# Kernel tuning notes

Hardware: AMD Instinct MI355X
Metric: run time of the kernel (lower is better)

The kernel has to match this reference:

```python
import jax, jax.numpy as jnp
import numpy as np

# Dimensions
B = 256        # number of graphs
NPG = 128      # nodes per graph (max_nodes; uniform -> to_dense_batch == reshape)
H = 8          # num_heads
DH = 32        # head_dim
HID = H * DH   # hidden_dim = 256
E = 524288     # n_edges
NGT = 20       # num_gate_types
EF = 8         # edge_feat_dim


def setup_inputs() -> dict:
    key = jax.random.key(0)
    ks = jax.random.split(key, 20)
    n_nodes = B * NPG
    x = jax.random.normal(ks[0], (n_nodes, HID), jnp.float32)
    # edges stay within the source node's graph
    src = jax.random.randint(ks[1], (E,), 0, n_nodes, dtype=jnp.int32)
    dst = (src // NPG) * NPG + jax.random.randint(ks[2], (E,), 0, NPG, dtype=jnp.int32)
    edge_index = jnp.stack([src, dst])  # [2, E]
    edge_attr = jax.random.normal(ks[3], (E, EF), jnp.float32)
    edge_gate_type = jax.random.randint(ks[4], (E,), 0, NGT, dtype=jnp.int32)
    batch = (jnp.arange(n_nodes) // NPG).astype(jnp.int32)

    s = 1.0 / np.sqrt(HID)
    def lin(k, din, dout, scale):
        kw, kb = jax.random.split(k)
        return (jax.random.uniform(kw, (din, dout), jnp.float32, -scale, scale),
                jax.random.uniform(kb, (dout,), jnp.float32, -scale, scale))
    Wq, bq = lin(ks[5], HID, HID, s)
    Wk, bk = lin(ks[6], HID, HID, s)
    Wv, bv = lin(ks[7], HID, HID, s)
    Wo, bo = lin(ks[8], HID, HID, s)
    gate_table = jax.random.normal(ks[9], (NGT, H), jnp.float32)
    We, be = lin(ks[10], EF, H, 1.0 / np.sqrt(EF))
    return {"x": x, "edge_attr": edge_attr, "Wq": Wq, "bq": bq, "Wk": Wk, "bk": bk,
            "Wv": Wv, "bv": bv, "Wo": Wo, "bo": bo, "gate_table": gate_table,
            "We": We, "be": be, "edge_index": edge_index,
            "edge_gate_type": edge_gate_type, "batch": batch}


def _edge_bias(edge_index, edge_attr, edge_gate_type, batch, gate_table, We, be):
    src, dst = edge_index[0], edge_index[1]
    eb = batch[src]                       # edge -> graph id
    src_l = src - eb * NPG                # local node index within graph
    dst_l = dst - eb * NPG
    total = gate_table[edge_gate_type] + edge_attr @ We + be   # [E, H]
    bias = jnp.zeros((B, H, NPG, NPG), edge_attr.dtype)
    bias = bias.at[eb, :, src_l, dst_l].add(total)             # forward direction
    rev = jnp.where((src_l != dst_l)[:, None], total, 0.0)     # skip self-loops
    bias = bias.at[eb, :, dst_l, src_l].add(rev)               # reverse direction
    return bias


def reference(x, edge_attr, Wq, bq, Wk, bk, Wv, bv, Wo, bo, gate_table, We, be,
              edge_index, edge_gate_type, batch):
    scale = 1.0 / np.sqrt(DH)
    xd = x.reshape(B, NPG, HID)  # uniform graph sizes -> to_dense_batch is a reshape
    Q = (xd @ Wq + bq).reshape(B, NPG, H, DH).transpose(0, 2, 1, 3)  # [B,H,N,D]
    K = (xd @ Wk + bk).reshape(B, NPG, H, DH).transpose(0, 2, 1, 3)
    V = (xd @ Wv + bv).reshape(B, NPG, H, DH).transpose(0, 2, 1, 3)
    scores = jnp.einsum('bhqd,bhkd->bhqk', Q, K) * scale
    scores = scores + _edge_bias(edge_index, edge_attr, edge_gate_type, batch,
                                 gate_table, We, be)
    attn = jax.nn.softmax(scores, axis=-1)  # node_mask all-True (uniform sizes)
    out = jnp.einsum('bhqk,bhkd->bhqd', attn, V)
    out = out.transpose(0, 2, 1, 3).reshape(B * NPG, HID)
    return out @ Wo + bo
```

## Files before the change

### kernel.cpp

```cpp
#include <hip/hip_runtime.h>
#include <hip/hip_fp16.h>

typedef unsigned short u16;
typedef unsigned int u32;
typedef __attribute__((ext_vector_type(8))) short short8;
typedef __attribute__((ext_vector_type(4))) float f32x4;

#define MFMA16(a, b, c) __builtin_amdgcn_mfma_f32_16x16x32_bf16((a), (b), (c), 0, 0, 0)

#define ESTRIDE 2304

__device__ __forceinline__ float b2f(u16 u) {
  union { float f; unsigned int i; } v;
  v.i = ((unsigned int)u) << 16;
  return v.f;
}
__device__ __forceinline__ u16 f2b(float f) {
  union { float f; unsigned int i; } v;
  v.f = f;
  unsigned int x = v.i;
  return (u16)((x + 0x7FFFu + ((x >> 16) & 1u)) >> 16);
}
__device__ __forceinline__ u16 f2h_bits(float f) {
  __half h = __float2half(f);
  u16 b;
  __builtin_memcpy(&b, &h, 2);
  return b;
}
__device__ __forceinline__ float h2f_bits(u16 b) {
  __half h;
  __builtin_memcpy(&h, &b, 2);
  return __half2float(h);
}

__device__ __forceinline__ void gload_lds16(const u16* g, u16* l) {
  __builtin_amdgcn_global_load_lds(
      (const __attribute__((address_space(1))) void*)g,
      (__attribute__((address_space(3))) void*)l, 16, 0, 0);
}

__global__ __launch_bounds__(256) void cvt_wtrans_kernel(
    const float* __restrict__ x, u16* __restrict__ xb,
    const float* __restrict__ W0, const float* __restrict__ W1,
    const float* __restrict__ W2, const float* __restrict__ W3,
    u16* __restrict__ T0, u16* __restrict__ T1,
    u16* __restrict__ T2, u16* __restrict__ T3) {
  int bx = blockIdx.x;
  if (bx < 4096) {
    size_t i = ((size_t)bx * 256 + threadIdx.x) * 8;
    const float4* p = (const float4*)(x + i);
    float4 v0 = p[0], v1 = p[1];
    float vf[8] = {v0.x, v0.y, v0.z, v0.w, v1.x, v1.y, v1.z, v1.w};
    short8 s;
#pragma unroll
    for (int j = 0; j < 8; ++j) s[j] = (short)f2b(vf[j]);
    *(short8*)(xb + i) = s;
  } else {
    int r = bx - 4096;
    const float* W; u16* T;
    switch (r >> 5) {
      case 0: W = W0; T = T0; break;
      case 1: W = W1; T = T1; break;
      case 2: W = W2; T = T2; break;
      default: W = W3; T = T3; break;
    }
    int n = threadIdx.x;
    int k0 = (r & 31) * 8;
    short8 s;
#pragma unroll
    for (int j = 0; j < 8; ++j) s[j] = (short)f2b(W[(size_t)(k0 + j) * 256 + n]);
    *(short8*)(T + (size_t)n * 256 + k0) = s;
  }
}

__global__ __launch_bounds__(256) void edge_build_kernel(
    const int* __restrict__ ei, const float* __restrict__ ea,
    const int* __restrict__ egt, const float* __restrict__ gate_table,
    const float* __restrict__ We, const float* __restrict__ be,
    u32* __restrict__ gfill, u16* __restrict__ etot16,
    u32* __restrict__ epos, int E) {
  __shared__ u32 hist[256];
  __shared__ u32 cursor[256];
  const int tid = threadIdx.x;
  hist[tid] = 0;
  __syncthreads();
  const int base_e = blockIdx.x * 2048;
  int gcache[8];
#pragma unroll
  for (int i = 0; i < 8; ++i) {
    int e = base_e + i * 256 + tid;
    int g = (e < E) ? (ei[e] >> 7) : -1;
    gcache[i] = g;
    if (g >= 0) atomicAdd(&hist[(u32)g], 1u);
  }
  __syncthreads();
  {
    u32 c = hist[tid];
    u32 r = c ? atomicAdd(&gfill[tid * 16], c) : 0u;
    cursor[tid] = (u32)tid * ESTRIDE + r;
  }
  __syncthreads();
#pragma unroll
  for (int i = 0; i < 8; ++i) {
    int g = gcache[i];
    if (g < 0) continue;
    int e = base_e + i * 256 + tid;
    int src = ei[e], dst = ei[E + e];
    int sl = src & 127, dl = dst & 127;
    int gt = egt[e];
    const float4* eap = (const float4*)(ea + (size_t)e * 8);
    float4 e0 = eap[0], e1 = eap[1];
    float eaf[8] = {e0.x, e0.y, e0.z, e0.w, e1.x, e1.y, e1.z, e1.w};
    short8 sv;
#pragma unroll
    for (int h = 0; h < 8; ++h) {
      float s = gate_table[gt * 8 + h] + be[h];
#pragma unroll
      for (int f = 0; f < 8; ++f) s += eaf[f] * We[f * 8 + h];
      sv[h] = (short)f2h_bits(s);
    }
    u32 pos = atomicAdd(&cursor[(u32)g], 1u);
    epos[pos] = (u32)sl | ((u32)dl << 16);
    *(short8*)(etot16 + (size_t)pos * 8) = sv;
  }
}

__global__ __launch_bounds__(256) void etrans_pad_kernel(
    const u16* __restrict__ aos, const u32* __restrict__ gfill,
    u16* __restrict__ soa, u32* __restrict__ epos) {
  int g = blockIdx.y;
  int p = blockIdx.x * 256 + threadIdx.x;
  u32 cnt = gfill[g * 16];
  size_t idx = (size_t)g * ESTRIDE + p;
  const size_t plane = (size_t)256 * ESTRIDE;
  if ((u32)p < cnt) {
    short8 v = *(const short8*)(aos + idx * 8);
#pragma unroll
    for (int h = 0; h < 8; ++h) soa[plane * h + idx] = (u16)v[h];
  } else {
    epos[idx] = 0;
#pragma unroll
    for (int h = 0; h < 8; ++h) soa[plane * h + idx] = 0;
  }
}

template <int NMAT, typename COUT>
__global__ __launch_bounds__(256) void gemm_tiled_kernel(
    const u16* __restrict__ A,
    const u16* __restrict__ T0, const u16* __restrict__ T1,
    const u16* __restrict__ T2,
    const float* __restrict__ b0, const float* __restrict__ b1,
    const float* __restrict__ b2,
    float s0, float s1, float s2,
    COUT* __restrict__ C0, COUT* __restrict__ C1, COUT* __restrict__ C2) {
  __shared__ __align__(16) u16 lA[128 * 64];
  __shared__ __align__(16) u16 lB[128 * 64];

  const int tid = threadIdx.x;
  const int bm = blockIdx.x;
  const int bn = blockIdx.y;
  const int m  = (NMAT == 1) ? 0 : (bn >> 1);
  const int ch = (NMAT == 1) ? bn : (bn & 1);

  const u16* Ts[3] = {T0, T1, T2};
  const float* bs[3] = {b0, b1, b2};
  const float scs[3] = {s0, s1, s2};
  COUT* Cs[3] = {C0, C1, C2};

  const u16* Abase = A + (size_t)(bm * 128) * 256;
  const u16* Bbase = Ts[m] + (size_t)(ch * 128) * 256;

  int srow[4];
  int selem[4];
#pragma unroll
  for (int i = 0; i < 4; ++i) {
    int c = i * 256 + tid;
    int row = c >> 3;
    int q = (c & 7) * 16;
    srow[i] = row;
    selem[i] = (q ^ ((row & 7) << 4)) >> 1;
  }

  const int wid = tid >> 6, lane = tid & 63;
  const int wm = wid >> 1, wn = wid & 1;
  const int quad = lane >> 4, l16 = lane & 15;
  const int swz = (l16 & 7) << 4;

  f32x4 acc[4][4] = {};

#pragma unroll
  for (int kt = 0; kt < 4; ++kt) {
    const int k0 = kt * 64;
    __syncthreads();
#pragma unroll
    for (int i = 0; i < 4; ++i) {
      gload_lds16(Abase + (size_t)srow[i] * 256 + k0 + selem[i],
                  lA + (size_t)(i * 256 + tid) * 8);
      gload_lds16(Bbase + (size_t)srow[i] * 256 + k0 + selem[i],
                  lB + (size_t)(i * 256 + tid) * 8);
    }
    __syncthreads();

#pragma unroll
    for (int ks = 0; ks < 2; ++ks) {
      const int kb = (ks * 64 + quad * 16) ^ swz;
      short8 af[4], bf[4];
#pragma unroll
      for (int i = 0; i < 4; ++i) {
        int arow = wm * 64 + i * 16 + l16;
        af[i] = *(const short8*)((const char*)lA + arow * 128 + kb);
        int brow = wn * 64 + i * 16 + l16;
        bf[i] = *(const short8*)((const char*)lB + brow * 128 + kb);
      }
#pragma unroll
      for (int i = 0; i < 4; ++i)
#pragma unroll
        for (int j = 0; j < 4; ++j)
          acc[i][j] = MFMA16(af[i], bf[j], acc[i][j]);
    }
  }

  const float* bias = bs[m];
  const float sc = scs[m];
  COUT* C = Cs[m];
#pragma unroll
  for (int j = 0; j < 4; ++j) {
    int col = ch * 128 + wn * 64 + j * 16 + l16;
    float bv = bias[col];
#pragma unroll
    for (int i = 0; i < 4; ++i) {
      int row0 = bm * 128 + wm * 64 + i * 16 + quad * 4;
#pragma unroll
      for (int r = 0; r < 4; ++r) {
        float o = (acc[i][j][r] + bv) * sc;
        if constexpr (sizeof(COUT) == 4)
          C[(size_t)(row0 + r) * 256 + col] = o;
        else
          C[(size_t)(row0 + r) * 256 + col] = f2b(o);
      }
    }
  }
}

__global__ __launch_bounds__(256) void attn_kernel(
    const u16* __restrict__ Q, const u16* __restrict__ K,
    const u16* __restrict__ V, const u32* __restrict__ epos,
    const u16* __restrict__ etot16, u16* __restrict__ O) {
  constexpr int LV = 144, LP = 136, LS = 132;
  constexpr int NE = ESTRIDE / 256;
  __shared__ __align__(16) char smem[33792];
  float* S   = (float*)smem;
  u16*   Pb  = (u16*)smem;
  u16*   Vt  = (u16*)(smem + 17408);
  float* inv = (float*)(smem + 26624);

  const int tid = threadIdx.x;
  const int qh = blockIdx.x, h = blockIdx.y, b = blockIdx.z;
  const int q0 = qh * 64;
  const int wid = tid >> 6, lane = tid & 63;
  const int quad = lane >> 4, l16 = lane & 15;

  u32 pd[NE]; u16 tb[NE];
  {
    const u32* ep = epos + (size_t)b * ESTRIDE + tid;
    const u16* ets = etot16 + (size_t)h * (256 * ESTRIDE) + (size_t)b * ESTRIDE + tid;
#pragma unroll
    for (int i = 0; i < NE; ++i) pd[i] = ep[i * 256];
#pragma unroll
    for (int i = 0; i < NE; ++i) tb[i] = ets[i * 256];
  }

  const int vr = tid >> 1, vs = (tid & 1) * 16;
  short8 vreg0, vreg1;
  {
    const u16* p = V + (size_t)(b * 128 + vr) * 256 + h * 32 + vs;
    vreg0 = *(const short8*)p;
    vreg1 = *(const short8*)(p + 8);
  }

  {
    short8 aq = *(const short8*)(
        Q + (size_t)(b * 128 + q0 + wid * 16 + l16) * 256 + h * 32 + quad * 8);
#pragma unroll
    for (int j = 0; j < 8; ++j) {
      short8 bk = *(const short8*)(
          K + (size_t)(b * 128 + j * 16 + l16) * 256 + h * 32 + quad * 8);
      f32x4 z = {0.f, 0.f, 0.f, 0.f};
      f32x4 sv = MFMA16(aq, bk, z);
#pragma unroll
      for (int r = 0; r < 4; ++r)
        S[(wid * 16 + quad * 4 + r) * LS + j * 16 + l16] = sv[r];
    }
  }
  __syncthreads();

#pragma unroll
  for (int i = 0; i < NE; ++i) {
    int sl = pd[i] & 0xffff, dl = pd[i] >> 16;
    float t = h2f_bits(tb[i]);
    int sr = sl - q0, dr = dl - q0;
    if ((unsigned)sr < 64u) atomicAdd(&S[sr * LS + dl], t);
    if (sl != dl && (unsigned)dr < 64u) atomicAdd(&S[dr * LS + sl], t);
  }
  __syncthreads();

  {
    int row = tid >> 2, c0 = (tid & 3) * 32;
    const float* srow = &S[row * LS + c0];
    float sv[32];
#pragma unroll
    for (int k = 0; k < 8; ++k) {
      float4 v = *(const float4*)(srow + k * 4);
      sv[k * 4 + 0] = v.x; sv[k * 4 + 1] = v.y;
      sv[k * 4 + 2] = v.z; sv[k * 4 + 3] = v.w;
    }
    float m = -1e30f;
#pragma unroll
    for (int c = 0; c < 32; ++c) m = fmaxf(m, sv[c]);
    m = fmaxf(m, __shfl_xor(m, 1, 64));
    m = fmaxf(m, __shfl_xor(m, 2, 64));
    float sum = 0.f;
    short8 prow[4];
#pragma unroll
    for (int c = 0; c < 32; ++c) {
      float p = __expf(sv[c] - m);
      sum += p;
      prow[c >> 3][c & 7] = (short)f2b(p);
    }
    sum += __shfl_xor(sum, 1, 64);
    sum += __shfl_xor(sum, 2, 64);
    __syncthreads();
#pragma unroll
    for (int k = 0; k < 4; ++k)
      *(short8*)&Pb[row * LP + c0 + k * 8] = prow[k];
#pragma unroll
    for (int j = 0; j < 8; ++j) {
      Vt[(vs + j) * LV + vr] = (u16)vreg0[j];
      Vt[(vs + 8 + j) * LV + vr] = (u16)vreg1[j];
    }
    if ((tid & 3) == 0) inv[row] = 1.f / sum;
  }
  __syncthreads();

  f32x4 oacc[2] = {};
#pragma unroll
  for (int ks = 0; ks < 4; ++ks) {
    short8 ap = *(short8*)&Pb[(wid * 16 + l16) * LP + ks * 32 + quad * 8];
#pragma unroll
    for (int j = 0; j < 2; ++j) {
      short8 bv = *(short8*)&Vt[(j * 16 + l16) * LV + ks * 32 + quad * 8];
      oacc[j] = MFMA16(ap, bv, oacc[j]);
    }
  }
#pragma unroll
  for (int j = 0; j < 2; ++j)
#pragma unroll
    for (int r = 0; r < 4; ++r) {
      int qr = wid * 16 + quad * 4 + r;
      float iv = inv[qr];
      O[(size_t)(b * 128 + q0 + qr) * 256 + h * 32 + j * 16 + l16] =
          f2b(oacc[j][r] * iv);
    }
}


extern "C" void kernel_launch(void* const* d_in, const int* in_sizes, int n_in,
                              void* d_out, int out_size, void* d_ws, size_t ws_size,
                              hipStream_t stream) {
  const float* x    = (const float*)d_in[0];
  const float* ea   = (const float*)d_in[1];
  const float* Wq   = (const float*)d_in[2];
  const float* bq   = (const float*)d_in[3];
  const float* Wk   = (const float*)d_in[4];
  const float* bk   = (const float*)d_in[5];
  const float* Wv   = (const float*)d_in[6];
  const float* bv   = (const float*)d_in[7];
  const float* Wo   = (const float*)d_in[8];
  const float* bo   = (const float*)d_in[9];
  const float* gate = (const float*)d_in[10];
  const float* We   = (const float*)d_in[11];
  const float* be   = (const float*)d_in[12];
  const int*   ei   = (const int*)d_in[13];
  const int*   egt  = (const int*)d_in[14];
  const int    E    = in_sizes[14];

  const size_t matBytes = (size_t)32768 * 256 * 2;
  const size_t slots = (size_t)256 * ESTRIDE;

  char* ws = (char*)d_ws;
  u16* Qm = (u16*)ws;
  u16* Km = (u16*)(ws + matBytes);
  u16* Vm = (u16*)(ws + 2 * matBytes);
  u16* Om = (u16*)(ws + 3 * matBytes);
  u16* xb = Om;
  u16*   etA  = (u16*)(ws + 4 * matBytes);
  u16*   etS  = etA + slots * 8;
  u32*   epos = (u32*)(etS + slots * 8);
  u32*   gfill = (u32*)((char*)epos + slots * 4);
  u16*   Wtq = (u16*)((char*)gfill + 4096 * 4);
  u16*   Wtk = Wtq + 65536;
  u16*   Wtv = Wtk + 65536;
  u16*   Wto = Wtv + 65536;

  hipMemsetAsync(gfill, 0, 4096 * sizeof(u32), stream);

  edge_build_kernel<<<dim3((E + 2047) / 2048), dim3(256), 0, stream>>>(
      ei, ea, egt, gate, We, be, gfill, etA, epos, E);
  etrans_pad_kernel<<<dim3(ESTRIDE / 256, 256), dim3(256), 0, stream>>>(
      etA, gfill, etS, epos);

  cvt_wtrans_kernel<<<dim3(4224), dim3(256), 0, stream>>>(
      x, xb, Wq, Wk, Wv, Wo, Wtq, Wtk, Wtv, Wto);

  const float qscale = 0.17677669529663687f;
  gemm_tiled_kernel<3, u16><<<dim3(256, 6), dim3(256), 0, stream>>>(
      xb, Wtq, Wtk, Wtv, bq, bk, bv, qscale, 1.f, 1.f, Qm, Km, Vm);

  attn_kernel<<<dim3(2, 8, 256), dim3(256), 0, stream>>>(
      Qm, Km, Vm, epos, etS, Om);

  gemm_tiled_kernel<1, float><<<dim3(256, 2), dim3(256), 0, stream>>>(
      Om, Wto, nullptr, nullptr, bo, nullptr, nullptr, 1.f, 1.f, 1.f,
      (float*)d_out, nullptr, nullptr);
}
```

Baseline: 256.2 us.

## Process full 128-row attention per block and swizzle score tile in LDS

The attention kernel now uses one 512-thread block per (head, graph) covering all 128 query rows instead of two 64-row halves. Each block therefore reads the per-graph edge list and edge biases once instead of twice, and the edge range checks are no longer needed. The score matrix in LDS gets an XOR column swizzle applied consistently on the QK^T writes, the atomic scatter and the softmax reads, to reduce bank conflicts. In exchange the kernel doubles its LDS use and launches half as many blocks, which may lower occupancy and parallelism.

```diff
diff --git a/kernel.cpp b/kernel.cpp
--- a/kernel.cpp
+++ b/kernel.cpp
@@ -242,75 +242,73 @@
   }
 }
 
-__global__ __launch_bounds__(256) void attn_kernel(
+__global__ __launch_bounds__(512) void attn_kernel(
     const u16* __restrict__ Q, const u16* __restrict__ K,
     const u16* __restrict__ V, const u32* __restrict__ epos,
     const u16* __restrict__ etot16, u16* __restrict__ O) {
   constexpr int LV = 144, LP = 136, LS = 132;
-  constexpr int NE = ESTRIDE / 256;
-  __shared__ __align__(16) char smem[33792];
+  __shared__ __align__(16) char smem[67584];
   float* S   = (float*)smem;
   u16*   Pb  = (u16*)smem;
-  u16*   Vt  = (u16*)(smem + 17408);
-  float* inv = (float*)(smem + 26624);
+  u16*   Vt  = (u16*)(smem + 34816);
+  float* inv = (float*)(smem + 44032);
 
   const int tid = threadIdx.x;
-  const int qh = blockIdx.x, h = blockIdx.y, b = blockIdx.z;
-  const int q0 = qh * 64;
+  const int h = blockIdx.x, b = blockIdx.y;
   const int wid = tid >> 6, lane = tid & 63;
   const int quad = lane >> 4, l16 = lane & 15;
 
-  u32 pd[NE]; u16 tb[NE];
+  u32 pd[5]; u16 tb[5];
   {
     const u32* ep = epos + (size_t)b * ESTRIDE + tid;
     const u16* ets = etot16 + (size_t)h * (256 * ESTRIDE) + (size_t)b * ESTRIDE + tid;
 #pragma unroll
-    for (int i = 0; i < NE; ++i) pd[i] = ep[i * 256];
-#pragma unroll
-    for (int i = 0; i < NE; ++i) tb[i] = ets[i * 256];
-  }
-
-  const int vr = tid >> 1, vs = (tid & 1) * 16;
-  short8 vreg0, vreg1;
-  {
-    const u16* p = V + (size_t)(b * 128 + vr) * 256 + h * 32 + vs;
-    vreg0 = *(const short8*)p;
-    vreg1 = *(const short8*)(p + 8);
-  }
+    for (int i = 0; i < 4; ++i) pd[i] = ep[i * 512];
+#pragma unroll
+    for (int i = 0; i < 4; ++i) tb[i] = ets[i * 512];
+    if (tid < 256) { pd[4] = ep[2048]; tb[4] = ets[2048]; }
+  }
+
+  const int vr = tid >> 2, vs = (tid & 3) * 8;
+  short8 vreg = *(const short8*)(V + (size_t)(b * 128 + vr) * 256 + h * 32 + vs);
 
   {
     short8 aq = *(const short8*)(
-        Q + (size_t)(b * 128 + q0 + wid * 16 + l16) * 256 + h * 32 + quad * 8);
+        Q + (size_t)(b * 128 + wid * 16 + l16) * 256 + h * 32 + quad * 8);
 #pragma unroll
     for (int j = 0; j < 8; ++j) {
       short8 bk = *(const short8*)(
           K + (size_t)(b * 128 + j * 16 + l16) * 256 + h * 32 + quad * 8);
       f32x4 z = {0.f, 0.f, 0.f, 0.f};
       f32x4 sv = MFMA16(aq, bk, z);
+      const int cswz = (j >> 1) << 3;
 #pragma unroll
       for (int r = 0; r < 4; ++r)
-        S[(wid * 16 + quad * 4 + r) * LS + j * 16 + l16] = sv[r];
-    }
-  }
-  __syncthreads();
-
-#pragma unroll
-  for (int i = 0; i < NE; ++i) {
-    int sl = pd[i] & 0xffff, dl = pd[i] >> 16;
-    float t = h2f_bits(tb[i]);
-    int sr = sl - q0, dr = dl - q0;
-    if ((unsigned)sr < 64u) atomicAdd(&S[sr * LS + dl], t);
-    if (sl != dl && (unsigned)dr < 64u) atomicAdd(&S[dr * LS + sl], t);
+        S[(wid * 16 + quad * 4 + r) * LS + ((j * 16 + l16) ^ cswz)] = sv[r];
+    }
+  }
+  __syncthreads();
+
+#pragma unroll
+  for (int i = 0; i < 5; ++i) {
+    if (i < 4 || tid < 256) {
+      int sl = pd[i] & 0xffff, dl = pd[i] >> 16;
+      float t = h2f_bits(tb[i]);
+      int dls = dl ^ ((dl & 0x60) >> 2);
+      int sls = sl ^ ((sl & 0x60) >> 2);
+      atomicAdd(&S[sl * LS + dls], t);
+      if (sl != dl) atomicAdd(&S[dl * LS + sls], t);
+    }
   }
   __syncthreads();
 
   {
-    int row = tid >> 2, c0 = (tid & 3) * 32;
-    const float* srow = &S[row * LS + c0];
+    int row = tid >> 2, t4 = tid & 3, c0 = t4 * 32;
+    const float* srow = &S[row * LS];
     float sv[32];
 #pragma unroll
     for (int k = 0; k < 8; ++k) {
-      float4 v = *(const float4*)(srow + k * 4);
+      float4 v = *(const float4*)(srow + ((c0 + k * 4) ^ (t4 << 3)));
       sv[k * 4 + 0] = v.x; sv[k * 4 + 1] = v.y;
       sv[k * 4 + 2] = v.z; sv[k * 4 + 3] = v.w;
     }
@@ -334,11 +332,9 @@
     for (int k = 0; k < 4; ++k)
       *(short8*)&Pb[row * LP + c0 + k * 8] = prow[k];
 #pragma unroll
-    for (int j = 0; j < 8; ++j) {
-      Vt[(vs + j) * LV + vr] = (u16)vreg0[j];
-      Vt[(vs + 8 + j) * LV + vr] = (u16)vreg1[j];
-    }
-    if ((tid & 3) == 0) inv[row] = 1.f / sum;
+    for (int j = 0; j < 8; ++j)
+      Vt[(vs + j) * LV + vr] = (u16)vreg[j];
+    if (t4 == 0) inv[row] = 1.f / sum;
   }
   __syncthreads();
 
@@ -358,7 +354,7 @@
     for (int r = 0; r < 4; ++r) {
       int qr = wid * 16 + quad * 4 + r;
       float iv = inv[qr];
-      O[(size_t)(b * 128 + q0 + qr) * 256 + h * 32 + j * 16 + l16] =
+      O[(size_t)(b * 128 + qr) * 256 + h * 32 + j * 16 + l16] =
           f2b(oacc[j][r] * iv);
     }
 }
@@ -416,7 +412,7 @@
   gemm_tiled_kernel<3, u16><<<dim3(256, 6), dim3(256), 0, stream>>>(
       xb, Wtq, Wtk, Wtv, bq, bk, bv, qscale, 1.f, 1.f, Qm, Km, Vm);
 
-  attn_kernel<<<dim3(2, 8, 256), dim3(256), 0, stream>>>(
+  attn_kernel<<<dim3(8, 256), dim3(512), 0, stream>>>(
       Qm, Km, Vm, epos, etS, Om);
 
   gemm_tiled_kernel<1, float><<<dim3(256, 2), dim3(256), 0, stream>>>(
```

Measured after the change: 261.1 us. About the same (+1.9%).

## Split attention into 32-row query tiles with smaller LDS and higher occupancy

Applied to the files above, without the earlier changes.

The attention kernel now processes 32 query rows per block instead of 64, doubling the grid. Shared memory shrinks to about 18KB and launch bounds request 8 blocks per CU. Warps are remapped so each computes half of the key columns for QK and one 16-column slice of the output for PV. The goal is more resident blocks to hide latency. The cost is that every block still reads all edge positions and biases and redundantly loads V and K for its (b,h), so edge loads and scan work per head double.

```diff
diff --git a/kernel.cpp b/kernel.cpp
--- a/kernel.cpp
+++ b/kernel.cpp
@@ -242,21 +242,21 @@
   }
 }
 
-__global__ __launch_bounds__(256) void attn_kernel(
+__global__ __launch_bounds__(256, 8) void attn_kernel(
     const u16* __restrict__ Q, const u16* __restrict__ K,
     const u16* __restrict__ V, const u32* __restrict__ epos,
     const u16* __restrict__ etot16, u16* __restrict__ O) {
   constexpr int LV = 144, LP = 136, LS = 132;
   constexpr int NE = ESTRIDE / 256;
-  __shared__ __align__(16) char smem[33792];
+  __shared__ __align__(16) char smem[18048];
   float* S   = (float*)smem;
   u16*   Pb  = (u16*)smem;
-  u16*   Vt  = (u16*)(smem + 17408);
-  float* inv = (float*)(smem + 26624);
+  u16*   Vt  = (u16*)(smem + 8704);
+  float* inv = (float*)(smem + 17920);
 
   const int tid = threadIdx.x;
-  const int qh = blockIdx.x, h = blockIdx.y, b = blockIdx.z;
-  const int q0 = qh * 64;
+  const int qq = blockIdx.x, h = blockIdx.y, b = blockIdx.z;
+  const int q0 = qq * 32;
   const int wid = tid >> 6, lane = tid & 63;
   const int quad = lane >> 4, l16 = lane & 15;
 
@@ -279,17 +279,18 @@
   }
 
   {
+    const int sr = (wid & 1) * 16, kh = (wid >> 1) * 64;
     short8 aq = *(const short8*)(
-        Q + (size_t)(b * 128 + q0 + wid * 16 + l16) * 256 + h * 32 + quad * 8);
-#pragma unroll
-    for (int j = 0; j < 8; ++j) {
+        Q + (size_t)(b * 128 + q0 + sr + l16) * 256 + h * 32 + quad * 8);
+#pragma unroll
+    for (int j = 0; j < 4; ++j) {
       short8 bk = *(const short8*)(
-          K + (size_t)(b * 128 + j * 16 + l16) * 256 + h * 32 + quad * 8);
+          K + (size_t)(b * 128 + kh + j * 16 + l16) * 256 + h * 32 + quad * 8);
       f32x4 z = {0.f, 0.f, 0.f, 0.f};
       f32x4 sv = MFMA16(aq, bk, z);
 #pragma unroll
       for (int r = 0; r < 4; ++r)
-        S[(wid * 16 + quad * 4 + r) * LS + j * 16 + l16] = sv[r];
+        S[(sr + quad * 4 + r) * LS + kh + j * 16 + l16] = sv[r];
     }
   }
   __syncthreads();
@@ -299,68 +300,68 @@
     int sl = pd[i] & 0xffff, dl = pd[i] >> 16;
     float t = h2f_bits(tb[i]);
     int sr = sl - q0, dr = dl - q0;
-    if ((unsigned)sr < 64u) atomicAdd(&S[sr * LS + dl], t);
-    if (sl != dl && (unsigned)dr < 64u) atomicAdd(&S[dr * LS + sl], t);
-  }
-  __syncthreads();
-
-  {
-    int row = tid >> 2, c0 = (tid & 3) * 32;
+    if ((unsigned)sr < 32u) atomicAdd(&S[sr * LS + dl], t);
+    if (sl != dl && (unsigned)dr < 32u) atomicAdd(&S[dr * LS + sl], t);
+  }
+  __syncthreads();
+
+  {
+    int row = tid >> 3, t8 = tid & 7, c0 = t8 * 16;
     const float* srow = &S[row * LS + c0];
-    float sv[32];
-#pragma unroll
-    for (int k = 0; k < 8; ++k) {
+    float sv[16];
+#pragma unroll
+    for (int k = 0; k < 4; ++k) {
       float4 v = *(const float4*)(srow + k * 4);
       sv[k * 4 + 0] = v.x; sv[k * 4 + 1] = v.y;
       sv[k * 4 + 2] = v.z; sv[k * 4 + 3] = v.w;
     }
     float m = -1e30f;
 #pragma unroll
-    for (int c = 0; c < 32; ++c) m = fmaxf(m, sv[c]);
+    for (int c = 0; c < 16; ++c) m = fmaxf(m, sv[c]);
     m = fmaxf(m, __shfl_xor(m, 1, 64));
     m = fmaxf(m, __shfl_xor(m, 2, 64));
+    m = fmaxf(m, __shfl_xor(m, 4, 64));
     float sum = 0.f;
-    short8 prow[4];
-#pragma unroll
-    for (int c = 0; c < 32; ++c) {
+    short8 prow[2];
+#pragma unroll
+    for (int c = 0; c < 16; ++c) {
       float p = __expf(sv[c] - m);
       sum += p;
       prow[c >> 3][c & 7] = (short)f2b(p);
     }
     sum += __shfl_xor(sum, 1, 64);
     sum += __shfl_xor(sum, 2, 64);
+    sum += __shfl_xor(sum, 4, 64);
     __syncthreads();
 #pragma unroll
-    for (int k = 0; k < 4; ++k)
+    for (int k = 0; k < 2; ++k)
       *(short8*)&Pb[row * LP + c0 + k * 8] = prow[k];
 #pragma unroll
     for (int j = 0; j < 8; ++j) {
       Vt[(vs + j) * LV + vr] = (u16)vreg0[j];
       Vt[(vs + 8 + j) * LV + vr] = (u16)vreg1[j];
     }
-    if ((tid & 3) == 0) inv[row] = 1.f / sum;
-  }
-  __syncthreads();
-
-  f32x4 oacc[2] = {};
-#pragma unroll
-  for (int ks = 0; ks < 4; ++ks) {
-    short8 ap = *(short8*)&Pb[(wid * 16 + l16) * LP + ks * 32 + quad * 8];
-#pragma unroll
-    for (int j = 0; j < 2; ++j) {
-      short8 bv = *(short8*)&Vt[(j * 16 + l16) * LV + ks * 32 + quad * 8];
-      oacc[j] = MFMA16(ap, bv, oacc[j]);
-    }
-  }
-#pragma unroll
-  for (int j = 0; j < 2; ++j)
+    if (t8 == 0) inv[row] = 1.f / sum;
+  }
+  __syncthreads();
+
+  {
+    const int s = (wid & 1) * 16, c = (wid >> 1) * 16;
+    f32x4 oacc = {};
+#pragma unroll
+    for (int ks = 0; ks < 4; ++ks) {
+      short8 ap = *(short8*)&Pb[(s + l16) * LP + ks * 32 + quad * 8];
+      short8 bv = *(short8*)&Vt[(c + l16) * LV + ks * 32 + quad * 8];
+      oacc = MFMA16(ap, bv, oacc);
+    }
 #pragma unroll
     for (int r = 0; r < 4; ++r) {
-      int qr = wid * 16 + quad * 4 + r;
+      int qr = s + quad * 4 + r;
       float iv = inv[qr];
-      O[(size_t)(b * 128 + q0 + qr) * 256 + h * 32 + j * 16 + l16] =
-          f2b(oacc[j][r] * iv);
-    }
+      O[(size_t)(b * 128 + q0 + qr) * 256 + h * 32 + c + l16] =
+          f2b(oacc[r] * iv);
+    }
+  }
 }
 
 
@@ -416,7 +417,7 @@
   gemm_tiled_kernel<3, u16><<<dim3(256, 6), dim3(256), 0, stream>>>(
       xb, Wtq, Wtk, Wtv, bq, bk, bv, qscale, 1.f, 1.f, Qm, Km, Vm);
 
-  attn_kernel<<<dim3(2, 8, 256), dim3(256), 0, stream>>>(
+  attn_kernel<<<dim3(4, 8, 256), dim3(256), 0, stream>>>(
       Qm, Km, Vm, epos, etS, Om);
 
   gemm_tiled_kernel<1, float><<<dim3(256, 2), dim3(256), 0, stream>>>(
```

Measured after the change: 262.1 us. 1.02x slower.
